# Kernel optimization log

Measured on AMD Instinct MI355X. Metric: run time of the kernel, lower is better.

## Reference

```python
import jax, jax.numpy as jnp
import numpy as np

# Irrep layout: 512x0e + 512x1o + 512x2e  (dims 512*1, 512*3, 512*5)
MUL = 512
LS = (0, 1, 2)


def setup_inputs() -> dict:
    key = jax.random.key(0)
    k1, k2, k3, k4 = jax.random.split(key, 4)
    N = 16384
    dim = MUL * sum(2 * l + 1 for l in LS)  # 4608
    x1 = jax.random.normal(k1, (N, dim), dtype=jnp.float32)
    x2 = jnp.ones((N, 1), dtype=jnp.float32)  # trivial 1x0e input of e3nn Linear
    W0 = jax.random.normal(k2, (MUL, 1, MUL), dtype=jnp.float32)
    W1 = jax.random.normal(k3, (MUL, 1, MUL), dtype=jnp.float32)
    W2 = jax.random.normal(k4, (MUL, 1, MUL), dtype=jnp.float32)
    return {"x1": x1, "x2": x2, "W0": W0, "W1": W1, "W2": W2}


def reference(x1, x2, W0, W1, W2):
    N = x1.shape[0]
    # path normalization: c = sqrt(alpha * path_weight / (mul_1 * mul_2)),
    # alpha = 1 (single path per output, unit variances), mul_2 = 1
    c = 1.0 / jnp.sqrt(jnp.asarray(MUL, dtype=x1.dtype))
    parts = []
    off = 0
    for W, l in ((W0, 0), (W1, 1), (W2, 2)):
        d = 2 * l + 1
        s1 = x1[:, off:off + MUL * d].reshape(N, MUL, d)  # [N, u, i]
        # specialized codegen branch (l2=0, l1=l_out, uvw):
        # out = c * einsum('uvw,zui,zv->zwi', ws, s1, s2)
        y = c * jnp.einsum('uvw,zui,zv->zwi', W, s1, x2)  # [N, w, i]
        parts.append(y.reshape(N, MUL * d))
        off += MUL * d
    return jnp.concatenate(parts, axis=1)
```

## Files before the change

### kernel.cpp

```cpp
#include <hip/hip_runtime.h>
#include <stdint.h>

typedef float f32x4 __attribute__((ext_vector_type(4)));
typedef __bf16 bf16x8 __attribute__((ext_vector_type(8)));
typedef unsigned short ushort4v __attribute__((ext_vector_type(4)));

#define DIM 4608
#define BK 32
#define NT 16
#define WS_L_BYTES (16 * 4 * 512 * 16)

#define BAR()                                    \
  do {                                           \
    __builtin_amdgcn_sched_barrier(0);           \
    asm volatile("s_waitcnt lgkmcnt(0)");        \
    __builtin_amdgcn_s_barrier();                \
    __builtin_amdgcn_sched_barrier(0);           \
  } while (0)

__global__ __launch_bounds__(256) void prepack(const float* __restrict__ W0,
                                               const float* __restrict__ W1,
                                               const float* __restrict__ W2,
                                               char* __restrict__ ws) {
  int gid = blockIdx.x * 256 + threadIdx.x;
  int col = gid & 511;
  int rest = gid >> 9;
  int grp = rest & 3;
  rest >>= 2;
  int t = rest & 15;
  int l = rest >> 4;
  const float* W = (l == 0) ? W0 : ((l == 1) ? W1 : W2);
  const float c = 0.044194173824159216f;
  union {
    bf16x8 v;
    uint4 u;
  } pk;
#pragma unroll
  for (int jj = 0; jj < 8; ++jj) {
    float v = W[(t * 32 + grp * 8 + jj) * 512 + col] * c;
    pk.v[jj] = (__bf16)v;
  }
  *(uint4*)(ws + (size_t)l * WS_L_BYTES + ((size_t)((t * 4 + grp) * 512 + col) << 4)) = pk.u;
}

template <int D, int BZ, int OFF>
__global__ __launch_bounds__(512) void gemm_l(const float* __restrict__ x1,
                                              const float* __restrict__ x2,
                                              const char* __restrict__ wsl,
                                              float* __restrict__ out) {
  constexpr int BM = BZ * D;
  constexpr int R = BM / 16;
  constexpr int ABYTES = BM * BK * 2;
  constexpr int CNT = BZ * 8 * D;
  constexpr int PF = (CNT + 511) / 512;

  __shared__ __align__(16) char smem[2 * ABYTES];

  const int tid = threadIdx.x;
  const int z0 = blockIdx.x * BZ;
  const float* xbase = x1 + (size_t)z0 * DIM + OFF;

  const int lane = tid & 63;
  const int wave = tid >> 6;
  const int llo = lane & 15;
  const int lhi = lane >> 4;

  f32x4 acc[R][4];
#pragma unroll
  for (int rt = 0; rt < R; ++rt)
#pragma unroll
    for (int ct = 0; ct < 4; ++ct) acc[rt][ct] = (f32x4){0.f, 0.f, 0.f, 0.f};

  auto load_a = [&](f32x4 (&pa)[PF], int t) {
    const float* xs = xbase + t * (BK * D);
#pragma unroll
    for (int s = 0; s < PF; ++s) {
      int idx = tid + s * 512;
      if (idx < CNT) {
        int zl = idx / (8 * D);
        int q = idx - zl * (8 * D);
        pa[s] = *(const f32x4*)(xs + (size_t)zl * DIM + q * 4);
      }
    }
  };

  auto load_b = [&](bf16x8 (&b)[4], int t) {
    const char* wt = wsl + (size_t)t * 32768;
#pragma unroll
    for (int ct = 0; ct < 4; ++ct)
      b[ct] = *(const bf16x8*)(wt + ((lhi * 512 + wave * 64 + ct * 16 + llo) << 4));
  };

  auto stage_write = [&](char* buf, f32x4 (&pa)[PF]) {
#pragma unroll
    for (int s = 0; s < PF; ++s) {
      int idx = tid + s * 512;
      if (idx < CNT) {
        int zl = idx / (8 * D);
        int q = idx - zl * (8 * D);
        if (D == 1) {
          int u0 = q * 4;
          union {
            ushort4v us;
            __bf16 b[4];
          } pk;
#pragma unroll
          for (int e = 0; e < 4; ++e) pk.b[e] = (__bf16)pa[s][e];
          *(ushort4v*)(buf + ((u0 >> 3) * BM + zl) * 16 + (u0 & 7) * 2) = pk.us;
        } else {
#pragma unroll
          for (int e = 0; e < 4; ++e) {
            int cl = q * 4 + e;
            int u = cl / D;
            int i = cl - u * D;
            int r = zl * D + i;
            *(__bf16*)(buf + ((u >> 3) * BM + r) * 16 + (u & 7) * 2) = (__bf16)pa[s][e];
          }
        }
      }
    }
  };

  auto compute = [&](const char* buf, bf16x8 (&b)[4]) {
#pragma unroll
    for (int rt = 0; rt < R; ++rt) {
      bf16x8 af = *(const bf16x8*)(buf + ((lhi * BM + rt * 16 + llo) << 4));
#pragma unroll
      for (int ct = 0; ct < 4; ++ct)
        acc[rt][ct] = __builtin_amdgcn_mfma_f32_16x16x32_bf16(af, b[ct], acc[rt][ct], 0, 0, 0);
    }
  };

  f32x4 paE[PF], paO[PF];
  bf16x8 bE[4], bO[4];
  load_a(paE, 0);
  load_b(bE, 0);
  load_a(paO, 1);
  load_b(bO, 1);
  stage_write(smem, paE);
  load_a(paE, 2);
  BAR();

#pragma unroll
  for (int tt = 0; tt < NT / 2; ++tt) {
    const int t = 2 * tt;
    compute(smem, bE);
    if (t + 2 < NT) load_b(bE, t + 2);
    stage_write(smem + ABYTES, paO);
    if (t + 3 < NT) load_a(paO, t + 3);
    BAR();
    compute(smem + ABYTES, bO);
    if (t + 3 < NT) load_b(bO, t + 3);
    if (t + 2 < NT) {
      stage_write(smem, paE);
      if (t + 4 < NT) load_a(paE, t + 4);
      BAR();
    }
  }

  float* obase = out + (size_t)z0 * DIM + OFF;
#pragma unroll
  for (int rt = 0; rt < R; ++rt) {
#pragma unroll
    for (int reg = 0; reg < 4; ++reg) {
      int row = rt * 16 + lhi * 4 + reg;
      int z = row / D;
      int i = row - z * D;
      float s = x2[z0 + z];
#pragma unroll
      for (int ct = 0; ct < 4; ++ct) {
        int col = wave * 64 + ct * 16 + llo;
        obase[(size_t)z * DIM + col * D + i] = acc[rt][ct][reg] * s;
      }
    }
  }
}

extern "C" void kernel_launch(void* const* d_in, const int* in_sizes, int n_in,
                              void* d_out, int out_size, void* d_ws, size_t ws_size,
                              hipStream_t stream) {
  const float* x1 = (const float*)d_in[0];
  const float* x2 = (const float*)d_in[1];
  const float* W0 = (const float*)d_in[2];
  const float* W1 = (const float*)d_in[3];
  const float* W2 = (const float*)d_in[4];
  float* out = (float*)d_out;
  char* ws = (char*)d_ws;

  prepack<<<384, 256, 0, stream>>>(W0, W1, W2, ws);
  gemm_l<1, 64, 0><<<256, 512, 0, stream>>>(x1, x2, ws, out);
  gemm_l<3, 16, 512><<<1024, 512, 0, stream>>>(x1, x2, ws + WS_L_BYTES, out);
  gemm_l<5, 16, 2048><<<1024, 512, 0, stream>>>(x1, x2, ws + 2 * WS_L_BYTES, out);
}
```

Baseline: 218.6 us.

## Fuse three per-irrep GEMM launches into one kernel and split output columns

Merges the three per-l GEMM kernels into one launch that dispatches on block index, with the heaviest l=2 blocks scheduled first. Each block now computes half of the 512 output columns, which doubles the grid and halves the accumulator registers; launch bounds request 4 blocks per CU. The aim is to remove launch gaps and tail effects and to improve occupancy. The cost is that every A tile is loaded and converted to bf16 twice, once per column half, which doubles x1 read traffic.

```diff
diff --git a/kernel.cpp b/kernel.cpp
--- a/kernel.cpp
+++ b/kernel.cpp
@@ -44,20 +44,20 @@
 }
 
 template <int D, int BZ, int OFF>
-__global__ __launch_bounds__(512) void gemm_l(const float* __restrict__ x1,
-                                              const float* __restrict__ x2,
-                                              const char* __restrict__ wsl,
-                                              float* __restrict__ out) {
+__device__ __forceinline__ void gemm_body(int lb, const float* __restrict__ x1,
+                                          const float* __restrict__ x2,
+                                          const char* __restrict__ wsl,
+                                          float* __restrict__ out,
+                                          char* __restrict__ smem) {
   constexpr int BM = BZ * D;
   constexpr int R = BM / 16;
-  constexpr int ABYTES = BM * BK * 2;
+  constexpr int ABYTES = BM * 64;
   constexpr int CNT = BZ * 8 * D;
   constexpr int PF = (CNT + 511) / 512;
 
-  __shared__ __align__(16) char smem[2 * ABYTES];
-
   const int tid = threadIdx.x;
-  const int z0 = blockIdx.x * BZ;
+  const int z0 = (lb >> 1) * BZ;
+  const int cb = (lb & 1) * 256;
   const float* xbase = x1 + (size_t)z0 * DIM + OFF;
 
   const int lane = tid & 63;
@@ -65,11 +65,11 @@
   const int llo = lane & 15;
   const int lhi = lane >> 4;
 
-  f32x4 acc[R][4];
+  f32x4 acc[R][2];
 #pragma unroll
   for (int rt = 0; rt < R; ++rt)
 #pragma unroll
-    for (int ct = 0; ct < 4; ++ct) acc[rt][ct] = (f32x4){0.f, 0.f, 0.f, 0.f};
+    for (int ct = 0; ct < 2; ++ct) acc[rt][ct] = (f32x4){0.f, 0.f, 0.f, 0.f};
 
   auto load_a = [&](f32x4 (&pa)[PF], int t) {
     const float* xs = xbase + t * (BK * D);
@@ -84,11 +84,11 @@
     }
   };
 
-  auto load_b = [&](bf16x8 (&b)[4], int t) {
+  auto load_b = [&](bf16x8 (&b)[2], int t) {
     const char* wt = wsl + (size_t)t * 32768;
 #pragma unroll
-    for (int ct = 0; ct < 4; ++ct)
-      b[ct] = *(const bf16x8*)(wt + ((lhi * 512 + wave * 64 + ct * 16 + llo) << 4));
+    for (int ct = 0; ct < 2; ++ct)
+      b[ct] = *(const bf16x8*)(wt + ((lhi * 512 + cb + wave * 32 + ct * 16 + llo) << 4));
   };
 
   auto stage_write = [&](char* buf, f32x4 (&pa)[PF]) {
@@ -121,18 +121,18 @@
     }
   };
 
-  auto compute = [&](const char* buf, bf16x8 (&b)[4]) {
+  auto compute = [&](const char* buf, bf16x8 (&b)[2]) {
 #pragma unroll
     for (int rt = 0; rt < R; ++rt) {
       bf16x8 af = *(const bf16x8*)(buf + ((lhi * BM + rt * 16 + llo) << 4));
 #pragma unroll
-      for (int ct = 0; ct < 4; ++ct)
+      for (int ct = 0; ct < 2; ++ct)
         acc[rt][ct] = __builtin_amdgcn_mfma_f32_16x16x32_bf16(af, b[ct], acc[rt][ct], 0, 0, 0);
     }
   };
 
   f32x4 paE[PF], paO[PF];
-  bf16x8 bE[4], bO[4];
+  bf16x8 bE[2], bO[2];
   load_a(paE, 0);
   load_b(bE, 0);
   load_a(paO, 1);
@@ -168,11 +168,26 @@
       int i = row - z * D;
       float s = x2[z0 + z];
 #pragma unroll
-      for (int ct = 0; ct < 4; ++ct) {
-        int col = wave * 64 + ct * 16 + llo;
+      for (int ct = 0; ct < 2; ++ct) {
+        int col = cb + wave * 32 + ct * 16 + llo;
         obase[(size_t)z * DIM + col * D + i] = acc[rt][ct][reg] * s;
       }
     }
+  }
+}
+
+__global__ __launch_bounds__(512, 4) void gemm_fused(const float* __restrict__ x1,
+                                                     const float* __restrict__ x2,
+                                                     const char* __restrict__ ws,
+                                                     float* __restrict__ out) {
+  __shared__ __align__(16) char smem[10240];
+  int bid = blockIdx.x;
+  if (bid < 2048) {
+    gemm_body<5, 16, 2048>(bid, x1, x2, ws + 2 * (size_t)WS_L_BYTES, out, smem);
+  } else if (bid < 4096) {
+    gemm_body<3, 16, 512>(bid - 2048, x1, x2, ws + (size_t)WS_L_BYTES, out, smem);
+  } else {
+    gemm_body<1, 64, 0>(bid - 4096, x1, x2, ws, out, smem);
   }
 }
 
@@ -188,7 +203,5 @@
   char* ws = (char*)d_ws;
 
   prepack<<<384, 256, 0, stream>>>(W0, W1, W2, ws);
-  gemm_l<1, 64, 0><<<256, 512, 0, stream>>>(x1, x2, ws, out);
-  gemm_l<3, 16, 512><<<1024, 512, 0, stream>>>(x1, x2, ws + WS_L_BYTES, out);
-  gemm_l<5, 16, 2048><<<1024, 512, 0, stream>>>(x1, x2, ws + 2 * WS_L_BYTES, out);
-}
+  gemm_fused<<<4608, 512, 0, stream>>>(x1, x2, ws, out);
+}
```

New measurement: 229.9 us. 5.1% more time.

## Split into bf16 transpose pre-pass and direct-load MFMA GEMM with chunking

Applied to the files above, without the earlier changes.

Adds an xpack kernel that scales x1 by x2, converts to bf16 and transposes it into a K-major workspace layout. A new LDS-free gemmx kernel then loads A and B fragments straight from global memory into MFMA. Work is chunked over N depending on workspace size, with the old fused kernel kept as fallback. This removes in-kernel staging and scatter into shared memory, at the cost of an extra full pass writing and re-reading an intermediate buffer.

```diff
diff --git a/kernel.cpp b/kernel.cpp
--- a/kernel.cpp
+++ b/kernel.cpp
@@ -6,17 +6,11 @@
 typedef unsigned short ushort4v __attribute__((ext_vector_type(4)));
 
 #define DIM 4608
-#define BK 32
-#define NT 16
+#define NZ 16384
 #define WS_L_BYTES (16 * 4 * 512 * 16)
-
-#define BAR()                                    \
-  do {                                           \
-    __builtin_amdgcn_sched_barrier(0);           \
-    asm volatile("s_waitcnt lgkmcnt(0)");        \
-    __builtin_amdgcn_s_barrier();                \
-    __builtin_amdgcn_sched_barrier(0);           \
-  } while (0)
+#define XT_OFF ((size_t)2 << 20)
+
+#define MFMA16 __builtin_amdgcn_mfma_f32_16x16x32_bf16
 
 __global__ __launch_bounds__(256) void prepack(const float* __restrict__ W0,
                                                const float* __restrict__ W1,
@@ -43,6 +37,91 @@
   *(uint4*)(ws + (size_t)l * WS_L_BYTES + ((size_t)((t * 4 + grp) * 512 + col) << 4)) = pk.u;
 }
 
+template <int D, int OFF>
+__global__ __launch_bounds__(256) void xpack(const float* __restrict__ x1,
+                                             const float* __restrict__ x2,
+                                             char* __restrict__ xt, int z0, int CZ) {
+  const int NRC = CZ * D;
+  int gid = blockIdx.x * 256 + threadIdx.x;
+  int tk = gid / NRC;
+  int rl = gid - tk * NRC;
+  int zl = rl / D;
+  int i = rl - zl * D;
+  const float* src = x1 + (size_t)(z0 + zl) * DIM + OFF + (tk * 8) * D + i;
+  float s = x2[z0 + zl];
+  union {
+    bf16x8 v;
+    uint4 u;
+  } pk;
+#pragma unroll
+  for (int j = 0; j < 8; ++j) pk.v[j] = (__bf16)(src[j * D] * s);
+  *(uint4*)(xt + ((size_t)tk * NRC + rl) * 16) = pk.u;
+}
+
+template <int D, int OFF>
+__global__ __launch_bounds__(512, 4) void gemmx(const char* __restrict__ xt,
+                                                const char* __restrict__ wsl,
+                                                float* __restrict__ out, int z0, int CZ) {
+  const int NRC = CZ * D;
+  const int tid = threadIdx.x;
+  const int lane = tid & 63;
+  const int wave = tid >> 6;
+  const int llo = lane & 15;
+  const int lhi = lane >> 4;
+  const int rbase = blockIdx.x * 64;
+  const int cb = wave * 64;
+
+  f32x4 acc[4][4];
+#pragma unroll
+  for (int rt = 0; rt < 4; ++rt)
+#pragma unroll
+    for (int ct = 0; ct < 4; ++ct) acc[rt][ct] = (f32x4){0.f, 0.f, 0.f, 0.f};
+
+  const char* abase = xt + ((size_t)lhi * NRC + rbase + llo) * 16;
+  const char* bbase = wsl + ((size_t)(lhi * 512 + cb + llo)) * 16;
+
+#pragma unroll
+  for (int kt = 0; kt < 16; ++kt) {
+    if ((kt & 3) == 0) __builtin_amdgcn_s_barrier();
+    bf16x8 a[4], b[4];
+#pragma unroll
+    for (int rt = 0; rt < 4; ++rt)
+      a[rt] = *(const bf16x8*)(abase + ((size_t)kt * 4 * NRC + rt * 16) * 16);
+#pragma unroll
+    for (int ct = 0; ct < 4; ++ct)
+      b[ct] = *(const bf16x8*)(bbase + ((size_t)kt * 4 * 512 + ct * 16) * 16);
+#pragma unroll
+    for (int rt = 0; rt < 4; ++rt)
+#pragma unroll
+      for (int ct = 0; ct < 4; ++ct)
+        acc[rt][ct] = MFMA16(a[rt], b[ct], acc[rt][ct], 0, 0, 0);
+  }
+
+#pragma unroll
+  for (int rt = 0; rt < 4; ++rt) {
+#pragma unroll
+    for (int reg = 0; reg < 4; ++reg) {
+      int row = rbase + rt * 16 + lhi * 4 + reg;
+      int z = row / D;
+      int i = row - z * D;
+      float* orow = out + (size_t)(z0 + z) * DIM + OFF + i;
+#pragma unroll
+      for (int ct = 0; ct < 4; ++ct) {
+        int col = cb + ct * 16 + llo;
+        orow[col * D] = acc[rt][ct][reg];
+      }
+    }
+  }
+}
+
+#define BAR()                                        \
+  do {                                               \
+    __builtin_amdgcn_sched_barrier(0);               \
+    asm volatile("s_waitcnt lgkmcnt(0)");            \
+    __builtin_amdgcn_s_barrier();                    \
+    __builtin_amdgcn_sched_barrier(0);               \
+  } while (0)
+
 template <int D, int BZ, int OFF>
 __global__ __launch_bounds__(512) void gemm_l(const float* __restrict__ x1,
                                               const float* __restrict__ x2,
@@ -50,29 +129,24 @@
                                               float* __restrict__ out) {
   constexpr int BM = BZ * D;
   constexpr int R = BM / 16;
-  constexpr int ABYTES = BM * BK * 2;
+  constexpr int ABYTES = BM * 64;
   constexpr int CNT = BZ * 8 * D;
   constexpr int PF = (CNT + 511) / 512;
-
   __shared__ __align__(16) char smem[2 * ABYTES];
-
   const int tid = threadIdx.x;
   const int z0 = blockIdx.x * BZ;
   const float* xbase = x1 + (size_t)z0 * DIM + OFF;
-
   const int lane = tid & 63;
   const int wave = tid >> 6;
   const int llo = lane & 15;
   const int lhi = lane >> 4;
-
   f32x4 acc[R][4];
 #pragma unroll
   for (int rt = 0; rt < R; ++rt)
 #pragma unroll
     for (int ct = 0; ct < 4; ++ct) acc[rt][ct] = (f32x4){0.f, 0.f, 0.f, 0.f};
-
-  auto load_a = [&](f32x4 (&pa)[PF], int t) {
-    const float* xs = xbase + t * (BK * D);
+  auto load_a = [&](f32x4(&pa)[PF], int t) {
+    const float* xs = xbase + t * (32 * D);
 #pragma unroll
     for (int s = 0; s < PF; ++s) {
       int idx = tid + s * 512;
@@ -83,15 +157,13 @@
       }
     }
   };
-
-  auto load_b = [&](bf16x8 (&b)[4], int t) {
+  auto load_b = [&](bf16x8(&b)[4], int t) {
     const char* wt = wsl + (size_t)t * 32768;
 #pragma unroll
     for (int ct = 0; ct < 4; ++ct)
       b[ct] = *(const bf16x8*)(wt + ((lhi * 512 + wave * 64 + ct * 16 + llo) << 4));
   };
-
-  auto stage_write = [&](char* buf, f32x4 (&pa)[PF]) {
+  auto stage_write = [&](char* buf, f32x4(&pa)[PF]) {
 #pragma unroll
     for (int s = 0; s < PF; ++s) {
       int idx = tid + s * 512;
@@ -102,10 +174,10 @@
           int u0 = q * 4;
           union {
             ushort4v us;
-            __bf16 b[4];
+            __bf16 b4[4];
           } pk;
 #pragma unroll
-          for (int e = 0; e < 4; ++e) pk.b[e] = (__bf16)pa[s][e];
+          for (int e = 0; e < 4; ++e) pk.b4[e] = (__bf16)pa[s][e];
           *(ushort4v*)(buf + ((u0 >> 3) * BM + zl) * 16 + (u0 & 7) * 2) = pk.us;
         } else {
 #pragma unroll
@@ -120,17 +192,15 @@
       }
     }
   };
-
-  auto compute = [&](const char* buf, bf16x8 (&b)[4]) {
+  auto compute = [&](const char* buf, bf16x8(&b)[4]) {
 #pragma unroll
     for (int rt = 0; rt < R; ++rt) {
       bf16x8 af = *(const bf16x8*)(buf + ((lhi * BM + rt * 16 + llo) << 4));
 #pragma unroll
       for (int ct = 0; ct < 4; ++ct)
-        acc[rt][ct] = __builtin_amdgcn_mfma_f32_16x16x32_bf16(af, b[ct], acc[rt][ct], 0, 0, 0);
-    }
-  };
-
+        acc[rt][ct] = MFMA16(af, b[ct], acc[rt][ct], 0, 0, 0);
+    }
+  };
   f32x4 paE[PF], paO[PF];
   bf16x8 bE[4], bO[4];
   load_a(paE, 0);
@@ -140,24 +210,22 @@
   stage_write(smem, paE);
   load_a(paE, 2);
   BAR();
-
-#pragma unroll
-  for (int tt = 0; tt < NT / 2; ++tt) {
+#pragma unroll
+  for (int tt = 0; tt < 8; ++tt) {
     const int t = 2 * tt;
     compute(smem, bE);
-    if (t + 2 < NT) load_b(bE, t + 2);
+    if (t + 2 < 16) load_b(bE, t + 2);
     stage_write(smem + ABYTES, paO);
-    if (t + 3 < NT) load_a(paO, t + 3);
+    if (t + 3 < 16) load_a(paO, t + 3);
     BAR();
     compute(smem + ABYTES, bO);
-    if (t + 3 < NT) load_b(bO, t + 3);
-    if (t + 2 < NT) {
+    if (t + 3 < 16) load_b(bO, t + 3);
+    if (t + 2 < 16) {
       stage_write(smem, paE);
-      if (t + 4 < NT) load_a(paE, t + 4);
+      if (t + 4 < 16) load_a(paE, t + 4);
       BAR();
     }
   }
-
   float* obase = out + (size_t)z0 * DIM + OFF;
 #pragma unroll
   for (int rt = 0; rt < R; ++rt) {
@@ -188,7 +256,29 @@
   char* ws = (char*)d_ws;
 
   prepack<<<384, 256, 0, stream>>>(W0, W1, W2, ws);
-  gemm_l<1, 64, 0><<<256, 512, 0, stream>>>(x1, x2, ws, out);
-  gemm_l<3, 16, 512><<<1024, 512, 0, stream>>>(x1, x2, ws + WS_L_BYTES, out);
-  gemm_l<5, 16, 2048><<<1024, 512, 0, stream>>>(x1, x2, ws + 2 * WS_L_BYTES, out);
-}
+
+  int CZ = 0;
+  for (int cz = NZ; cz >= 2048; cz >>= 1)
+    if (XT_OFF + (size_t)cz * 9216 <= ws_size) {
+      CZ = cz;
+      break;
+    }
+
+  if (CZ) {
+    char* xt0 = ws + XT_OFF;
+    char* xt1 = xt0 + (size_t)CZ * 1024;
+    char* xt2 = xt1 + (size_t)CZ * 3072;
+    for (int z0 = 0; z0 < NZ; z0 += CZ) {
+      xpack<1, 0><<<CZ * 1 / 4, 256, 0, stream>>>(x1, x2, xt0, z0, CZ);
+      xpack<3, 512><<<CZ * 3 / 4, 256, 0, stream>>>(x1, x2, xt1, z0, CZ);
+      xpack<5, 2048><<<CZ * 5 / 4, 256, 0, stream>>>(x1, x2, xt2, z0, CZ);
+      gemmx<1, 0><<<CZ * 1 / 64, 512, 0, stream>>>(xt0, ws, out, z0, CZ);
+      gemmx<3, 512><<<CZ * 3 / 64, 512, 0, stream>>>(xt1, ws + WS_L_BYTES, out, z0, CZ);
+      gemmx<5, 2048><<<CZ * 5 / 64, 512, 0, stream>>>(xt2, ws + 2 * (size_t)WS_L_BYTES, out, z0, CZ);
+    }
+  } else {
+    gemm_l<1, 64, 0><<<256, 512, 0, stream>>>(x1, x2, ws, out);
+    gemm_l<3, 16, 512><<<1024, 512, 0, stream>>>(x1, x2, ws + WS_L_BYTES, out);
+    gemm_l<5, 16, 2048><<<1024, 512, 0, stream>>>(x1, x2, ws + 2 * (size_t)WS_L_BYTES, out);
+  }
+}
```

Measured after the change: 407.6 us. 1.86x slower.
